# Kernel optimization log

Hardware: AMD Instinct MI355X
Metric: run time of the kernel (lower is better)

## Reference

```python
import jax, jax.numpy as jnp
import numpy as np

D_MODEL = 1024
N_HEADS = 16
D_HEAD = D_MODEL // N_HEADS
ROPE_BASE = 10000.0
B, L = 2, 2048


def setup_inputs() -> dict:
    key = jax.random.key(0)
    k1, k2, k3 = jax.random.split(key, 3)
    x = jax.random.normal(k1, (B, L, D_MODEL), dtype=jnp.float32)
    W_qkv = jax.random.normal(k2, (3 * D_MODEL, D_MODEL), dtype=jnp.float32) * (1.0 / np.sqrt(D_MODEL))
    W_out = jax.random.normal(k3, (D_MODEL, D_MODEL), dtype=jnp.float32) * (1.0 / np.sqrt(D_MODEL))
    position_ids = jnp.broadcast_to(jnp.arange(L, dtype=jnp.int32), (B, L))
    attn_mask_2d = jnp.broadcast_to(jnp.tril(jnp.ones((L, L), dtype=bool)), (B, L, L))
    return {"x": x, "W_qkv": W_qkv, "W_out": W_out,
            "position_ids": position_ids, "attn_mask_2d": attn_mask_2d}


def _apply_rope(t, position_ids, inv_freq):
    # t: (B, H, L, Dh) float32; position_ids: (B, L) int
    f = position_ids.astype(jnp.float32)[:, :, None] * inv_freq  # (B, L, Dh/2)
    cos = jnp.cos(f)[:, None]  # (B, 1, L, Dh/2)
    sin = jnp.sin(f)[:, None]
    x1 = t[..., 0::2]
    x2 = t[..., 1::2]
    rot_even = x1 * cos - x2 * sin
    rot_odd = x1 * sin + x2 * cos
    return jnp.stack((rot_even, rot_odd), axis=-1).reshape(t.shape)


def reference(x, W_qkv, W_out, position_ids, attn_mask_2d):
    Bb, Ll, D = x.shape
    H, Dh = N_HEADS, D // N_HEADS
    inv_freq = 1.0 / (ROPE_BASE ** (jnp.arange(0, Dh, 2, dtype=jnp.float32) / Dh))  # (Dh/2,)
    qkv = jnp.einsum('bld,ed->ble', x, W_qkv).reshape(Bb, Ll, 3, H, Dh)
    qkv = jnp.transpose(qkv, (2, 0, 3, 1, 4))  # (3, B, H, L, Dh)
    q, k, v = qkv[0], qkv[1], qkv[2]
    q = _apply_rope(q.astype(jnp.float32), position_ids, inv_freq).astype(x.dtype)
    k = _apply_rope(k.astype(jnp.float32), position_ids, inv_freq).astype(x.dtype)
    scale = 1.0 / np.sqrt(Dh).astype(np.float32)
    scores = jnp.einsum('bhld,bhmd->bhlm', q, k) * scale  # (B, H, L, L)
    neg = jnp.finfo(scores.dtype).min
    scores = jnp.where(attn_mask_2d[:, None], scores, neg)
    attn = jax.nn.softmax(scores, axis=-1)
    out = jnp.einsum('bhlm,bhmd->bhld', attn, v)
    out = jnp.transpose(out, (0, 2, 1, 3)).reshape(Bb, Ll, D)
    return jnp.einsum('bld,ed->ble', out, W_out)
```

## Files before the change

kernel.cpp:

```cpp
#include <hip/hip_runtime.h>
#include <hip/hip_bf16.h>
#include <math.h>

typedef float f32x4 __attribute__((ext_vector_type(4)));
typedef __bf16 bf16x8 __attribute__((ext_vector_type(8)));

__device__ inline f32x4 mfma16(bf16x8 a, bf16x8 b, f32x4 c) {
    return __builtin_amdgcn_mfma_f32_16x16x32_bf16(a, b, c, 0, 0, 0);
}
__device__ inline unsigned short f2bf(float f) {
    union { float f; unsigned u; } v; v.f = f;
    unsigned r = v.u + 0x7fffu + ((v.u >> 16) & 1u);
    return (unsigned short)(r >> 16);
}
__device__ inline float bf2f(unsigned short b) {
    union { unsigned u; float f; } v; v.u = ((unsigned)b) << 16;
    return v.f;
}
__device__ inline unsigned pack2(float a, float b) {
    return (unsigned)f2bf(a) | ((unsigned)f2bf(b) << 16);
}
__device__ inline f32x4 vzero() { f32x4 z = {0.f, 0.f, 0.f, 0.f}; return z; }

#define GLD16(gptr, lptr)                                                            \
    __builtin_amdgcn_global_load_lds(                                                \
        (const __attribute__((address_space(1))) unsigned int*)(const void*)(gptr),  \
        (__attribute__((address_space(3))) unsigned int*)(void*)(lptr), 16, 0, 0)

__global__ __launch_bounds__(256)
void convert_xw(const float* __restrict__ x, const float* __restrict__ wqkv,
                unsigned short* __restrict__ xb, unsigned short* __restrict__ wqkvb)
{
    int i = blockIdx.x * 256 + threadIdx.x;
    const float* src; unsigned short* dst; int off;
    if (i < 524288) { src = x;    dst = xb;    off = i; }
    else            { src = wqkv; dst = wqkvb; off = i - 524288; }
    const float4* p = (const float4*)src + (size_t)off * 2;
    float4 f0 = p[0], f1 = p[1];
    uint4 o;
    o.x = pack2(f0.x, f0.y); o.y = pack2(f0.z, f0.w);
    o.z = pack2(f1.x, f1.y); o.w = pack2(f1.z, f1.w);
    ((uint4*)dst)[off] = o;
}

template<int MI, int C32, int WPB>
__global__ __launch_bounds__(256, WPB)
void gemm_bt(const unsigned short* __restrict__ A,
             const unsigned short* __restrict__ Wt,
             void* __restrict__ C_, int M, int N, int K)
{
    __shared__ __align__(16) unsigned short As[MI * 32 * 64];
    __shared__ __align__(16) unsigned short Bs[128 * 64];

    const int tid  = threadIdx.x;
    const int wave = tid >> 6;
    const int lane = tid & 63;
    const int quad = lane >> 4;
    const int c0   = lane & 15;
    const int m0 = blockIdx.y * (MI * 32);
    const int n0 = blockIdx.x * 128;
    const int wm = (wave >> 1) * (MI * 16);
    const int wn = (wave & 1) * 64;

    const int lrow   = lane >> 3;
    const int gchunk = (lane & 7) ^ lrow;
    const int goff   = gchunk * 8;

    f32x4 acc[MI][4];
#pragma unroll
    for (int i = 0; i < MI; i++)
#pragma unroll
        for (int j = 0; j < 4; j++) acc[i][j] = vzero();

    for (int k0 = 0; k0 < K; k0 += 64) {
        __syncthreads();
#pragma unroll
        for (int p = 0; p < MI; p++) {
            int r0 = p * 32 + wave * 8;
            GLD16(&A[(size_t)(m0 + r0 + lrow) * K + k0 + goff], &As[r0 * 64]);
        }
#pragma unroll
        for (int p = 0; p < 4; p++) {
            int r0 = p * 32 + wave * 8;
            GLD16(&Wt[(size_t)(n0 + r0 + lrow) * K + k0 + goff], &Bs[r0 * 64]);
        }
        __syncthreads();
#pragma unroll
        for (int kk = 0; kk < 2; kk++) {
            const int pos = ((kk * 4 + quad) ^ (c0 & 7)) * 8;
            bf16x8 af[MI], bfr[4];
#pragma unroll
            for (int i = 0; i < MI; i++)
                af[i] = *(const bf16x8*)&As[(wm + i * 16 + c0) * 64 + pos];
#pragma unroll
            for (int j = 0; j < 4; j++)
                bfr[j] = *(const bf16x8*)&Bs[(wn + j * 16 + c0) * 64 + pos];
#pragma unroll
            for (int i = 0; i < MI; i++)
#pragma unroll
                for (int j = 0; j < 4; j++)
                    acc[i][j] = mfma16(af[i], bfr[j], acc[i][j]);
        }
    }

#pragma unroll
    for (int i = 0; i < MI; i++)
#pragma unroll
        for (int j = 0; j < 4; j++)
#pragma unroll
            for (int r = 0; r < 4; r++) {
                int row  = m0 + wm + i * 16 + quad * 4 + r;
                int colg = n0 + wn + j * 16 + c0;
                if (C32) ((float*)C_)[(size_t)row * N + colg] = acc[i][j][r];
                else ((unsigned short*)C_)[(size_t)row * N + colg] = f2bf(acc[i][j][r]);
            }
}

__global__ __launch_bounds__(256)
void rope_vtrans(const unsigned short* __restrict__ qkv,
                 const int* __restrict__ pos,
                 unsigned short* __restrict__ Qb,
                 unsigned short* __restrict__ Kb,
                 unsigned short* __restrict__ Vt,
                 const float* __restrict__ wout,
                 unsigned short* __restrict__ woutb)
{
    __shared__ unsigned short T[256 * 64];
    const int id = blockIdx.x;
    if (id < 8192) {
        int tid = id * 256 + threadIdx.x;
        int d2 = tid & 31;
        int h  = (tid >> 5) & 15;
        int l  = (tid >> 9) & 2047;
        int b  = tid >> 20;
        size_t row = (size_t)(b * 2048 + l) * 3072;
        int col = h * 64 + 2 * d2;
        float inv_freq = exp2f((float)(-2 * d2) * (13.287712379549449f / 64.0f));
        float f = (float)pos[b * 2048 + l] * inv_freq;
        float s, c;
        sincosf(f, &s, &c);
        unsigned qw = *(const unsigned*)&qkv[row + col];
        unsigned kw = *(const unsigned*)&qkv[row + 1024 + col];
        float q1 = bf2f((unsigned short)qw), q2 = bf2f((unsigned short)(qw >> 16));
        float k1 = bf2f((unsigned short)kw), k2 = bf2f((unsigned short)(kw >> 16));
        const float qs = 0.18033688011112042f;
        size_t o = ((size_t)((b * 16 + h) * 2048 + l)) * 64 + 2 * d2;
        *(unsigned*)&Qb[o] = pack2((q1 * c - q2 * s) * qs, (q1 * s + q2 * c) * qs);
        *(unsigned*)&Kb[o] = pack2(k1 * c - k2 * s, k1 * s + k2 * c);
    } else if (id < 8448) {
        const int id2 = id - 8192;
        const int t = threadIdx.x;
        const int l0 = (id2 & 7) * 256, h = (id2 >> 3) & 15, b = id2 >> 7;
#pragma unroll
        for (int i = 0; i < 8; i++) {
            int c = t + i * 256;
            int r = c >> 3, c8 = c & 7;
            int p = (c8 + (r >> 3)) & 7;
            *(uint4*)&T[r * 64 + p * 8] =
                *(const uint4*)&qkv[(size_t)(b * 2048 + l0 + r) * 3072 + 2048 + h * 64 + c8 * 8];
        }
        __syncthreads();
#pragma unroll
        for (int i = 0; i < 8; i++) {
            int c = t + i * 256;
            int dh = c >> 5, lc = c & 31;
            int blk = dh >> 3;
            unsigned short tmp[8];
#pragma unroll
            for (int j = 0; j < 8; j++) {
                int l = lc * 8 + j;
                int p = (blk + lc) & 7;
                tmp[j] = T[l * 64 + p * 8 + (dh & 7)];
            }
            *(uint4*)&Vt[((size_t)(b * 16 + h) * 64 + dh) * 2048 + l0 + lc * 8] = *(uint4*)tmp;
        }
    } else {
        int i = (id - 8448) * 256 + threadIdx.x;
        const float4* p = (const float4*)wout + (size_t)i * 2;
        float4 f0 = p[0], f1 = p[1];
        uint4 o;
        o.x = pack2(f0.x, f0.y); o.y = pack2(f0.z, f0.w);
        o.z = pack2(f1.x, f1.y); o.w = pack2(f1.z, f1.w);
        ((uint4*)woutb)[i] = o;
    }
}

__global__ __launch_bounds__(256, 2)
void attn(const unsigned short* __restrict__ Q,
          const unsigned short* __restrict__ Kb,
          const unsigned short* __restrict__ Vt,
          unsigned short* __restrict__ O)
{
    __shared__ unsigned short QsA[64 * 64];
    __shared__ unsigned short QsB[64 * 64];
    __shared__ unsigned short Ks[64 * 64];
    __shared__ unsigned short Vts[64 * 64];
    __shared__ unsigned short PsA[64 * 64];
    __shared__ unsigned short PsB[64 * 64];

    const int tid  = threadIdx.x;
    const int wave = tid >> 6;
    const int lane = tid & 63;
    const int quad = lane >> 4;
    const int c0   = lane & 15;
    const int id = blockIdx.x;
    const int jp = id >> 5;
    const int h  = id & 15;
    const int b  = (id >> 4) & 1;
    const int qtA = jp, qtB = 31 - jp;
    const size_t headoff = ((size_t)(b * 16 + h)) * 2048 * 64;
    const int q0A = qtA * 64, q0B = qtB * 64;
    const float C = 11.541560327111707f;

    const int ca = tid, cb2 = tid + 256;
    const int ra = ca >> 3, c8a = ca & 7;
    const int rb = cb2 >> 3, c8b = cb2 & 7;
    const int la = ra * 64 + (c8a ^ (ra & 7)) * 8;
    const int lb = rb * 64 + (c8b ^ (rb & 7)) * 8;

    bf16x8 ones;
#pragma unroll
    for (int j = 0; j < 8; j++) ones[j] = (__bf16)1.0f;

    uint4 kreg0, kreg1, vreg0, vreg1;
    {
        kreg0 = *(const uint4*)&Kb[headoff + (size_t)ra * 64 + c8a * 8];
        kreg1 = *(const uint4*)&Kb[headoff + (size_t)rb * 64 + c8b * 8];
        vreg0 = *(const uint4*)&Vt[headoff + (size_t)ra * 2048 + c8a * 8];
        vreg1 = *(const uint4*)&Vt[headoff + (size_t)rb * 2048 + c8b * 8];
    }
    *(uint4*)&QsA[la] = *(const uint4*)&Q[headoff + (size_t)(q0A + ra) * 64 + c8a * 8];
    *(uint4*)&QsA[lb] = *(const uint4*)&Q[headoff + (size_t)(q0A + rb) * 64 + c8b * 8];
    *(uint4*)&QsB[la] = *(const uint4*)&Q[headoff + (size_t)(q0B + ra) * 64 + c8a * 8];
    *(uint4*)&QsB[lb] = *(const uint4*)&Q[headoff + (size_t)(q0B + rb) * 64 + c8b * 8];

    f32x4 oA[4], oB[4];
#pragma unroll
    for (int j = 0; j < 4; j++) { oA[j] = vzero(); oB[j] = vzero(); }
    f32x4 laccA = vzero(), laccB = vzero();

    for (int kt = 0; kt <= qtB; kt++) {
        __syncthreads();
        *(uint4*)&Ks[la] = kreg0;
        *(uint4*)&Ks[lb] = kreg1;
        *(uint4*)&Vts[la] = vreg0;
        *(uint4*)&Vts[lb] = vreg1;
        __syncthreads();
        if (kt < qtB) {
            size_t k1o = headoff + (size_t)(kt + 1) * 4096;
            kreg0 = *(const uint4*)&Kb[k1o + (size_t)ra * 64 + c8a * 8];
            kreg1 = *(const uint4*)&Kb[k1o + (size_t)rb * 64 + c8b * 8];
            vreg0 = *(const uint4*)&Vt[headoff + (size_t)ra * 2048 + (kt + 1) * 64 + c8a * 8];
            vreg1 = *(const uint4*)&Vt[headoff + (size_t)rb * 2048 + (kt + 1) * 64 + c8b * 8];
        }
        const bool doA = (kt <= qtA);

        {
            f32x4 s[4];
#pragma unroll
            for (int nj = 0; nj < 4; nj++) s[nj] = vzero();
#pragma unroll
            for (int kk = 0; kk < 2; kk++) {
                const int pos = ((kk * 4 + quad) ^ (c0 & 7)) * 8;
                bf16x8 aq = *(const bf16x8*)&QsB[(wave * 16 + c0) * 64 + pos];
#pragma unroll
                for (int nj = 0; nj < 4; nj++) {
                    bf16x8 bk = *(const bf16x8*)&Ks[(nj * 16 + c0) * 64 + pos];
                    s[nj] = mfma16(aq, bk, s[nj]);
                }
            }
            if (kt == qtB) {
#pragma unroll
                for (int nj = 0; nj < 4; nj++)
#pragma unroll
                    for (int r = 0; r < 4; r++) {
                        int key  = nj * 16 + c0;
                        int qrow = wave * 16 + quad * 4 + r;
                        if (key > qrow) s[nj][r] = -1e38f;
                    }
            }
#pragma unroll
            for (int nj = 0; nj < 4; nj++)
#pragma unroll
                for (int r = 0; r < 4; r++) {
                    union { float f; unsigned u; } pv;
                    pv.f = __builtin_amdgcn_exp2f(s[nj][r] - C);
                    int row = wave * 16 + quad * 4 + r;
                    int col = nj * 16 + c0;
                    int pp = ((col >> 3) + row) & 7;
                    PsB[row * 64 + pp * 8 + (col & 7)] = (unsigned short)(pv.u >> 16);
                }
        }
        if (doA) {
            f32x4 s[4];
#pragma unroll
            for (int nj = 0; nj < 4; nj++) s[nj] = vzero();
#pragma unroll
            for (int kk = 0; kk < 2; kk++) {
                const int pos = ((kk * 4 + quad) ^ (c0 & 7)) * 8;
                bf16x8 aq = *(const bf16x8*)&QsA[(wave * 16 + c0) * 64 + pos];
#pragma unroll
                for (int nj = 0; nj < 4; nj++) {
                    bf16x8 bk = *(const bf16x8*)&Ks[(nj * 16 + c0) * 64 + pos];
                    s[nj] = mfma16(aq, bk, s[nj]);
                }
            }
            if (kt == qtA) {
#pragma unroll
                for (int nj = 0; nj < 4; nj++)
#pragma unroll
                    for (int r = 0; r < 4; r++) {
                        int key  = nj * 16 + c0;
                        int qrow = wave * 16 + quad * 4 + r;
                        if (key > qrow) s[nj][r] = -1e38f;
                    }
            }
#pragma unroll
            for (int nj = 0; nj < 4; nj++)
#pragma unroll
                for (int r = 0; r < 4; r++) {
                    union { float f; unsigned u; } pv;
                    pv.f = __builtin_amdgcn_exp2f(s[nj][r] - C);
                    int row = wave * 16 + quad * 4 + r;
                    int col = nj * 16 + c0;
                    int pp = ((col >> 3) + row) & 7;
                    PsA[row * 64 + pp * 8 + (col & 7)] = (unsigned short)(pv.u >> 16);
                }
        }
        __syncthreads();

#pragma unroll
        for (int kk = 0; kk < 2; kk++) {
            const int pos = ((kk * 4 + quad) ^ (c0 & 7)) * 8;
            int prow = wave * 16 + c0;
            int pp = ((kk * 4 + quad) + prow) & 7;
            bf16x8 ap = *(const bf16x8*)&PsB[prow * 64 + pp * 8];
            laccB = mfma16(ap, ones, laccB);
#pragma unroll
            for (int cj = 0; cj < 4; cj++) {
                bf16x8 bv = *(const bf16x8*)&Vts[(cj * 16 + c0) * 64 + pos];
                oB[cj] = mfma16(ap, bv, oB[cj]);
            }
        }
        if (doA) {
#pragma unroll
            for (int kk = 0; kk < 2; kk++) {
                const int pos = ((kk * 4 + quad) ^ (c0 & 7)) * 8;
                int prow = wave * 16 + c0;
                int pp = ((kk * 4 + quad) + prow) & 7;
                bf16x8 ap = *(const bf16x8*)&PsA[prow * 64 + pp * 8];
                laccA = mfma16(ap, ones, laccA);
#pragma unroll
                for (int cj = 0; cj < 4; cj++) {
                    bf16x8 bv = *(const bf16x8*)&Vts[(cj * 16 + c0) * 64 + pos];
                    oA[cj] = mfma16(ap, bv, oA[cj]);
                }
            }
        }
    }

#pragma unroll
    for (int r = 0; r < 4; r++) {
        float invA = 1.0f / laccA[r];
        float invB = 1.0f / laccB[r];
        int qlA = q0A + wave * 16 + quad * 4 + r;
        int qlB = q0B + wave * 16 + quad * 4 + r;
        size_t baseA = ((size_t)b * 2048 + qlA) * 1024 + h * 64;
        size_t baseB = ((size_t)b * 2048 + qlB) * 1024 + h * 64;
#pragma unroll
        for (int cj = 0; cj < 4; cj++) {
            O[baseA + cj * 16 + c0] = f2bf(oA[cj][r] * invA);
            O[baseB + cj * 16 + c0] = f2bf(oB[cj][r] * invB);
        }
    }
}

extern "C" void kernel_launch(void* const* d_in, const int* in_sizes, int n_in,
                              void* d_out, int out_size, void* d_ws, size_t ws_size,
                              hipStream_t stream) {
    const int* pos = (const int*)d_in[3];

    unsigned short* regA = (unsigned short*)d_ws;
    unsigned short* regB = regA + (size_t)4096 * 1024;
    unsigned short* regC = regB + (size_t)4096 * 1024;
    unsigned short* regD = regC + (size_t)4096 * 1024;
    unsigned short* regE = regD + (size_t)4096 * 3072;

    unsigned short* xb    = regA;
    unsigned short* wqkvb = regB;
    unsigned short* qkv   = regD;
    unsigned short* Qb    = regA;
    unsigned short* Kb    = regB;
    unsigned short* Vt    = regC;
    unsigned short* Ob    = regD;
    unsigned short* woutb = regE;

    convert_xw<<<3584, 256, 0, stream>>>((const float*)d_in[0], (const float*)d_in[1],
                                         xb, wqkvb);
    gemm_bt<4, 0, 4><<<dim3(24, 32), 256, 0, stream>>>(xb, wqkvb, qkv, 4096, 3072, 1024);
    rope_vtrans<<<8960, 256, 0, stream>>>(qkv, pos, Qb, Kb, Vt,
                                          (const float*)d_in[2], woutb);
    attn<<<512, 256, 0, stream>>>(Qb, Kb, Vt, Ob);
    gemm_bt<2, 1, 3><<<dim3(8, 64), 256, 0, stream>>>(Ob, woutb, d_out, 4096, 1024, 1024);
}
```

Measured before the change: 194.0 us.

## Process two K/V tiles per barrier and use wave-local waits for P

The attention loop now stages two 64-key K/V tiles per iteration into double-buffered shared memory and prefetches the next two tiles into registers. The workgroup barrier between writing and reading the softmax P tile is replaced by an lgkmcnt wait. Each wave only reads the P rows it wrote itself, so that wait is sufficient. The aim is to cut workgroup barriers per key tile and deepen global-load prefetch, at the cost of more registers and shared memory, which could lower occupancy.

```diff
diff --git a/kernel.cpp b/kernel.cpp
--- a/kernel.cpp
+++ b/kernel.cpp
@@ -193,8 +193,8 @@
 {
     __shared__ unsigned short QsA[64 * 64];
     __shared__ unsigned short QsB[64 * 64];
-    __shared__ unsigned short Ks[64 * 64];
-    __shared__ unsigned short Vts[64 * 64];
+    __shared__ unsigned short Ks[2][64 * 64];
+    __shared__ unsigned short Vts[2][64 * 64];
     __shared__ unsigned short PsA[64 * 64];
     __shared__ unsigned short PsB[64 * 64];
 
@@ -222,12 +222,14 @@
 #pragma unroll
     for (int j = 0; j < 8; j++) ones[j] = (__bf16)1.0f;
 
-    uint4 kreg0, kreg1, vreg0, vreg1;
-    {
-        kreg0 = *(const uint4*)&Kb[headoff + (size_t)ra * 64 + c8a * 8];
-        kreg1 = *(const uint4*)&Kb[headoff + (size_t)rb * 64 + c8b * 8];
-        vreg0 = *(const uint4*)&Vt[headoff + (size_t)ra * 2048 + c8a * 8];
-        vreg1 = *(const uint4*)&Vt[headoff + (size_t)rb * 2048 + c8b * 8];
+    uint4 kr[2][2], vr[2][2];
+#pragma unroll
+    for (int t = 0; t < 2; t++) {
+        size_t ko = headoff + (size_t)t * 4096;
+        kr[t][0] = *(const uint4*)&Kb[ko + (size_t)ra * 64 + c8a * 8];
+        kr[t][1] = *(const uint4*)&Kb[ko + (size_t)rb * 64 + c8b * 8];
+        vr[t][0] = *(const uint4*)&Vt[headoff + (size_t)ra * 2048 + t * 64 + c8a * 8];
+        vr[t][1] = *(const uint4*)&Vt[headoff + (size_t)rb * 2048 + t * 64 + c8b * 8];
     }
     *(uint4*)&QsA[la] = *(const uint4*)&Q[headoff + (size_t)(q0A + ra) * 64 + c8a * 8];
     *(uint4*)&QsA[lb] = *(const uint4*)&Q[headoff + (size_t)(q0A + rb) * 64 + c8b * 8];
@@ -239,121 +241,141 @@
     for (int j = 0; j < 4; j++) { oA[j] = vzero(); oB[j] = vzero(); }
     f32x4 laccA = vzero(), laccB = vzero();
 
-    for (int kt = 0; kt <= qtB; kt++) {
+    for (int kt = 0; kt <= qtB; kt += 2) {
+        const bool has2 = (kt + 1 <= qtB);
         __syncthreads();
-        *(uint4*)&Ks[la] = kreg0;
-        *(uint4*)&Ks[lb] = kreg1;
-        *(uint4*)&Vts[la] = vreg0;
-        *(uint4*)&Vts[lb] = vreg1;
+        *(uint4*)&Ks[0][la] = kr[0][0];
+        *(uint4*)&Ks[0][lb] = kr[0][1];
+        *(uint4*)&Vts[0][la] = vr[0][0];
+        *(uint4*)&Vts[0][lb] = vr[0][1];
+        if (has2) {
+            *(uint4*)&Ks[1][la] = kr[1][0];
+            *(uint4*)&Ks[1][lb] = kr[1][1];
+            *(uint4*)&Vts[1][la] = vr[1][0];
+            *(uint4*)&Vts[1][lb] = vr[1][1];
+        }
         __syncthreads();
-        if (kt < qtB) {
-            size_t k1o = headoff + (size_t)(kt + 1) * 4096;
-            kreg0 = *(const uint4*)&Kb[k1o + (size_t)ra * 64 + c8a * 8];
-            kreg1 = *(const uint4*)&Kb[k1o + (size_t)rb * 64 + c8b * 8];
-            vreg0 = *(const uint4*)&Vt[headoff + (size_t)ra * 2048 + (kt + 1) * 64 + c8a * 8];
-            vreg1 = *(const uint4*)&Vt[headoff + (size_t)rb * 2048 + (kt + 1) * 64 + c8b * 8];
-        }
-        const bool doA = (kt <= qtA);
-
-        {
-            f32x4 s[4];
-#pragma unroll
-            for (int nj = 0; nj < 4; nj++) s[nj] = vzero();
-#pragma unroll
-            for (int kk = 0; kk < 2; kk++) {
-                const int pos = ((kk * 4 + quad) ^ (c0 & 7)) * 8;
-                bf16x8 aq = *(const bf16x8*)&QsB[(wave * 16 + c0) * 64 + pos];
-#pragma unroll
-                for (int nj = 0; nj < 4; nj++) {
-                    bf16x8 bk = *(const bf16x8*)&Ks[(nj * 16 + c0) * 64 + pos];
-                    s[nj] = mfma16(aq, bk, s[nj]);
-                }
-            }
-            if (kt == qtB) {
+        if (kt + 2 <= qtB) {
+            size_t ko = headoff + (size_t)(kt + 2) * 4096;
+            kr[0][0] = *(const uint4*)&Kb[ko + (size_t)ra * 64 + c8a * 8];
+            kr[0][1] = *(const uint4*)&Kb[ko + (size_t)rb * 64 + c8b * 8];
+            vr[0][0] = *(const uint4*)&Vt[headoff + (size_t)ra * 2048 + (kt + 2) * 64 + c8a * 8];
+            vr[0][1] = *(const uint4*)&Vt[headoff + (size_t)rb * 2048 + (kt + 2) * 64 + c8b * 8];
+        }
+        if (kt + 3 <= qtB) {
+            size_t ko = headoff + (size_t)(kt + 3) * 4096;
+            kr[1][0] = *(const uint4*)&Kb[ko + (size_t)ra * 64 + c8a * 8];
+            kr[1][1] = *(const uint4*)&Kb[ko + (size_t)rb * 64 + c8b * 8];
+            vr[1][0] = *(const uint4*)&Vt[headoff + (size_t)ra * 2048 + (kt + 3) * 64 + c8a * 8];
+            vr[1][1] = *(const uint4*)&Vt[headoff + (size_t)rb * 2048 + (kt + 3) * 64 + c8b * 8];
+        }
+
+#pragma unroll
+        for (int t = 0; t < 2; t++) {
+            if (t == 1 && !has2) break;
+            const int cur = kt + t;
+            const bool doA = (cur <= qtA);
+
+            {
+                f32x4 s[4];
+#pragma unroll
+                for (int nj = 0; nj < 4; nj++) s[nj] = vzero();
+#pragma unroll
+                for (int kk = 0; kk < 2; kk++) {
+                    const int pos = ((kk * 4 + quad) ^ (c0 & 7)) * 8;
+                    bf16x8 aq = *(const bf16x8*)&QsB[(wave * 16 + c0) * 64 + pos];
+#pragma unroll
+                    for (int nj = 0; nj < 4; nj++) {
+                        bf16x8 bk = *(const bf16x8*)&Ks[t][(nj * 16 + c0) * 64 + pos];
+                        s[nj] = mfma16(aq, bk, s[nj]);
+                    }
+                }
+                if (cur == qtB) {
+#pragma unroll
+                    for (int nj = 0; nj < 4; nj++)
+#pragma unroll
+                        for (int r = 0; r < 4; r++) {
+                            int key  = nj * 16 + c0;
+                            int qrow = wave * 16 + quad * 4 + r;
+                            if (key > qrow) s[nj][r] = -1e38f;
+                        }
+                }
 #pragma unroll
                 for (int nj = 0; nj < 4; nj++)
 #pragma unroll
                     for (int r = 0; r < 4; r++) {
-                        int key  = nj * 16 + c0;
-                        int qrow = wave * 16 + quad * 4 + r;
-                        if (key > qrow) s[nj][r] = -1e38f;
+                        union { float f; unsigned u; } pv;
+                        pv.f = __builtin_amdgcn_exp2f(s[nj][r] - C);
+                        int row = wave * 16 + quad * 4 + r;
+                        int col = nj * 16 + c0;
+                        int pp = ((col >> 3) + row) & 7;
+                        PsB[row * 64 + pp * 8 + (col & 7)] = (unsigned short)(pv.u >> 16);
                     }
             }
-#pragma unroll
-            for (int nj = 0; nj < 4; nj++)
-#pragma unroll
-                for (int r = 0; r < 4; r++) {
-                    union { float f; unsigned u; } pv;
-                    pv.f = __builtin_amdgcn_exp2f(s[nj][r] - C);
-                    int row = wave * 16 + quad * 4 + r;
-                    int col = nj * 16 + c0;
-                    int pp = ((col >> 3) + row) & 7;
-                    PsB[row * 64 + pp * 8 + (col & 7)] = (unsigned short)(pv.u >> 16);
-                }
-        }
-        if (doA) {
-            f32x4 s[4];
-#pragma unroll
-            for (int nj = 0; nj < 4; nj++) s[nj] = vzero();
-#pragma unroll
-            for (int kk = 0; kk < 2; kk++) {
-                const int pos = ((kk * 4 + quad) ^ (c0 & 7)) * 8;
-                bf16x8 aq = *(const bf16x8*)&QsA[(wave * 16 + c0) * 64 + pos];
-#pragma unroll
-                for (int nj = 0; nj < 4; nj++) {
-                    bf16x8 bk = *(const bf16x8*)&Ks[(nj * 16 + c0) * 64 + pos];
-                    s[nj] = mfma16(aq, bk, s[nj]);
-                }
-            }
-            if (kt == qtA) {
+            if (doA) {
+                f32x4 s[4];
+#pragma unroll
+                for (int nj = 0; nj < 4; nj++) s[nj] = vzero();
+#pragma unroll
+                for (int kk = 0; kk < 2; kk++) {
+                    const int pos = ((kk * 4 + quad) ^ (c0 & 7)) * 8;
+                    bf16x8 aq = *(const bf16x8*)&QsA[(wave * 16 + c0) * 64 + pos];
+#pragma unroll
+                    for (int nj = 0; nj < 4; nj++) {
+                        bf16x8 bk = *(const bf16x8*)&Ks[t][(nj * 16 + c0) * 64 + pos];
+                        s[nj] = mfma16(aq, bk, s[nj]);
+                    }
+                }
+                if (cur == qtA) {
+#pragma unroll
+                    for (int nj = 0; nj < 4; nj++)
+#pragma unroll
+                        for (int r = 0; r < 4; r++) {
+                            int key  = nj * 16 + c0;
+                            int qrow = wave * 16 + quad * 4 + r;
+                            if (key > qrow) s[nj][r] = -1e38f;
+                        }
+                }
 #pragma unroll
                 for (int nj = 0; nj < 4; nj++)
 #pragma unroll
                     for (int r = 0; r < 4; r++) {
-                        int key  = nj * 16 + c0;
-                        int qrow = wave * 16 + quad * 4 + r;
-                        if (key > qrow) s[nj][r] = -1e38f;
+                        union { float f; unsigned u; } pv;
+                        pv.f = __builtin_amdgcn_exp2f(s[nj][r] - C);
+                        int row = wave * 16 + quad * 4 + r;
+                        int col = nj * 16 + c0;
+                        int pp = ((col >> 3) + row) & 7;
+                        PsA[row * 64 + pp * 8 + (col & 7)] = (unsigned short)(pv.u >> 16);
                     }
             }
-#pragma unroll
-            for (int nj = 0; nj < 4; nj++)
-#pragma unroll
-                for (int r = 0; r < 4; r++) {
-                    union { float f; unsigned u; } pv;
-                    pv.f = __builtin_amdgcn_exp2f(s[nj][r] - C);
-                    int row = wave * 16 + quad * 4 + r;
-                    int col = nj * 16 + c0;
-                    int pp = ((col >> 3) + row) & 7;
-                    PsA[row * 64 + pp * 8 + (col & 7)] = (unsigned short)(pv.u >> 16);
-                }
-        }
-        __syncthreads();
-
-#pragma unroll
-        for (int kk = 0; kk < 2; kk++) {
-            const int pos = ((kk * 4 + quad) ^ (c0 & 7)) * 8;
-            int prow = wave * 16 + c0;
-            int pp = ((kk * 4 + quad) + prow) & 7;
-            bf16x8 ap = *(const bf16x8*)&PsB[prow * 64 + pp * 8];
-            laccB = mfma16(ap, ones, laccB);
-#pragma unroll
-            for (int cj = 0; cj < 4; cj++) {
-                bf16x8 bv = *(const bf16x8*)&Vts[(cj * 16 + c0) * 64 + pos];
-                oB[cj] = mfma16(ap, bv, oB[cj]);
-            }
-        }
-        if (doA) {
+            asm volatile("s_waitcnt lgkmcnt(0)" ::: "memory");
+
 #pragma unroll
             for (int kk = 0; kk < 2; kk++) {
                 const int pos = ((kk * 4 + quad) ^ (c0 & 7)) * 8;
                 int prow = wave * 16 + c0;
                 int pp = ((kk * 4 + quad) + prow) & 7;
-                bf16x8 ap = *(const bf16x8*)&PsA[prow * 64 + pp * 8];
-                laccA = mfma16(ap, ones, laccA);
+                bf16x8 ap = *(const bf16x8*)&PsB[prow * 64 + pp * 8];
+                laccB = mfma16(ap, ones, laccB);
 #pragma unroll
                 for (int cj = 0; cj < 4; cj++) {
-                    bf16x8 bv = *(const bf16x8*)&Vts[(cj * 16 + c0) * 64 + pos];
-                    oA[cj] = mfma16(ap, bv, oA[cj]);
+                    bf16x8 bv = *(const bf16x8*)&Vts[t][(cj * 16 + c0) * 64 + pos];
+                    oB[cj] = mfma16(ap, bv, oB[cj]);
+                }
+            }
+            if (doA) {
+#pragma unroll
+                for (int kk = 0; kk < 2; kk++) {
+                    const int pos = ((kk * 4 + quad) ^ (c0 & 7)) * 8;
+                    int prow = wave * 16 + c0;
+                    int pp = ((kk * 4 + quad) + prow) & 7;
+                    bf16x8 ap = *(const bf16x8*)&PsA[prow * 64 + pp * 8];
+                    laccA = mfma16(ap, ones, laccA);
+#pragma unroll
+                    for (int cj = 0; cj < 4; cj++) {
+                        bf16x8 bv = *(const bf16x8*)&Vts[t][(cj * 16 + c0) * 64 + pos];
+                        oA[cj] = mfma16(ap, bv, oA[cj]);
+                    }
                 }
             }
         }
```

Result: slower. 224.5 us (+15.7%).
